# Kernel optimization log

Hardware: AMD Instinct MI355X
Metric: run time of the kernel (lower is better)

The kernel has to match this reference:

```python
import jax, jax.numpy as jnp
import numpy as np

# Intrinsics from innerProdLoss defaults
FX, FY, CX, CY = 48.0, 48.0, 48.0, 36.0
H, W = int(2 * CY), int(2 * CX)  # 72, 96
N = H * W                         # 6912 pixels
SIGMA2 = 1.0                      # geometric Gaussian-kernel bandwidth (reconstructed kern_mat)
EPS = 1e-8


def make_yz1_grid():
    # K = [[cx,fx,0],[cy,0,fy],[1,0,0]]; yz1_grid = inv(K) @ uv1_grid, shape [3, N]
    K = np.array([[CX, FX, 0.0], [CY, 0.0, FY], [1.0, 0.0, 0.0]], dtype=np.float64)
    invK = np.linalg.inv(K).astype(np.float32)
    u = np.arange(W, dtype=np.float32)
    v = np.arange(H, dtype=np.float32)
    uu = np.tile(u[None, :], (H, 1)).reshape(-1)
    vv = np.tile(v[:, None], (1, W)).reshape(-1)
    uv1 = np.stack([uu, vv, np.ones_like(uu)], axis=0)  # [3, N]
    return jnp.asarray(invK @ uv1)

YZ1 = make_yz1_grid()  # [3, N]


def kern_mat(p1, p2):
    # p1, p2: [B, 3, N] point clouds -> [B, N, N] Gaussian kernel exp(-||d||^2 / (2 sigma^2)).
    # Squared distances via norms + cross term (no [B,3,N,N] diff tensor).
    n1 = jnp.sum(p1 * p1, axis=1)                    # [B, N]
    n2 = jnp.sum(p2 * p2, axis=1)                    # [B, N]
    cross = jnp.einsum('bcm,bcn->bmn', p1, p2)       # [B, N, N]
    d2 = jnp.maximum(n1[:, :, None] + n2[:, None, :] - 2.0 * cross, 0.0)
    return jnp.exp(-d2 / (2.0 * SIGMA2))


def gramian(f1, f2):
    # f1, f2: [B, C, H, W] -> gramian [B, N, N] of L2-normalized features (norm_mode=1, kernalize=False).
    B, C, Hh, Ww = f1.shape
    n = Hh * Ww
    f1 = f1.reshape(B, C, n)
    f2 = f2.reshape(B, C, n)
    norm1 = jnp.linalg.norm(f1, axis=1)              # [B, N]
    norm2 = jnp.linalg.norm(f2, axis=1)
    fea_norm_sum = jnp.sum(norm1) + jnp.sum(norm2)
    f1n = f1 / (norm1[:, None, :] + EPS)
    f2n = f2 / (norm2[:, None, :] + EPS)
    gram = jnp.einsum('bcm,bcn->bmn', f1n, f2n) / n  # norm_mode=1 normalization
    return gram, fea_norm_sum


def setup_inputs() -> dict:
    key = jax.random.key(0)
    k1, k2, k3, k4, k5 = jax.random.split(key, 5)
    B, C = 1, 16
    feature1 = jax.random.normal(k1, (B, C, H, W), jnp.float32)
    feature2 = jax.random.normal(k2, (B, C, H, W), jnp.float32)
    depth1 = jax.random.uniform(k3, (B, 1, H, W), jnp.float32, 0.5, 5.0)
    depth2 = jax.random.uniform(k4, (B, 1, H, W), jnp.float32, 0.5, 5.0)
    pose1_2 = jnp.tile(jnp.eye(4, dtype=jnp.float32)[None], (B, 1, 1))
    pose_noise = jnp.eye(4, dtype=jnp.float32) + 0.01 * jax.random.normal(k5, (4, 4), jnp.float32)
    return {"feature1": feature1, "feature2": feature2, "depth1": depth1,
            "depth2": depth2, "pose1_2": pose1_2, "pose_noise": pose_noise}


def reference(feature1, feature2, depth1, depth2, pose1_2, pose_noise):
    B = depth1.shape[0]
    # gen_3D: back-project pixels using depth
    xyz1 = YZ1[None] * depth1.reshape(B, 1, N)       # [B, 3, N]
    xyz2 = YZ1[None] * depth2.reshape(B, 1, N)
    xyz2_homo = jnp.concatenate([xyz2, jnp.ones((B, 1, N), xyz2.dtype)], axis=1)  # [B, 4, N]
    xyz2_trans = jnp.matmul(pose1_2, xyz2_homo)[:, :3, :]

    gram_feat, fea_norm_sum = gramian(feature1, feature2)
    pcl_diff_exp = kern_mat(xyz1, xyz2_trans)

    # L2_norm=True, diff_mode=True -> scale by 100
    fea_norm_sum = fea_norm_sum * 100.0

    # diff_mode: noisy pose branch
    pose_noisy = jnp.matmul(pose1_2, pose_noise)
    xyz2_trans_noisy = jnp.matmul(pose_noisy, xyz2_homo)[:, :3, :]
    pcl_diff_exp_noisy = kern_mat(xyz1, xyz2_trans_noisy)

    inner_neg = -jnp.sum((pcl_diff_exp - pcl_diff_exp_noisy) * gram_feat)
    final_loss = inner_neg  # sparse_mode=False
    return final_loss, inner_neg, fea_norm_sum
```

## Files before the change

### kernel.cpp

```cpp
#include <hip/hip_runtime.h>
#include <math.h>

#define NPIX 6912
#define LOG2E 1.4426950408889634f

typedef __fp16 v8h  __attribute__((ext_vector_type(8)));
typedef float  v16f __attribute__((ext_vector_type(16)));

#define OFF_ROWFEAT 0
#define OFF_ROWGEO  221184
#define OFF_COLFEAT 442368
#define OFF_COLB1   663552
#define OFF_COLB2   884736
#define OFF_PART    1105920
#define OFF_NPART   1117584
#define NPART_BLOCKS 2916
#define NNORM_BLOCKS 108

__device__ __forceinline__ float fast_exp2(float x) { return __builtin_amdgcn_exp2f(x); }

__device__ __forceinline__ float wave_reduce_64(float v) {
    #pragma unroll
    for (int o = 32; o > 0; o >>= 1) v += __shfl_down(v, o, 64);
    return v;
}

__device__ __forceinline__ float block_reduce_256(float v, float* smem4) {
    __syncthreads();
    v = wave_reduce_64(v);
    const int lane = threadIdx.x & 63;
    const int w = threadIdx.x >> 6;
    if (lane == 0) smem4[w] = v;
    __syncthreads();
    float r = 0.0f;
    if (threadIdx.x == 0) r = smem4[0] + smem4[1] + smem4[2] + smem4[3];
    return r;
}

__device__ __forceinline__ void split_hl(float x, __fp16& h, __fp16& l) {
    h = (__fp16)x;
    l = (__fp16)(x - (float)h);
}

__global__ __launch_bounds__(64)
void preproc_kernel(const float* __restrict__ f1, const float* __restrict__ f2,
                    const float* __restrict__ d1, const float* __restrict__ d2,
                    const float* __restrict__ pose, const float* __restrict__ pnz,
                    char* __restrict__ wsb) {
    const int i = blockIdx.x * 64 + threadIdx.x;

    __fp16* rowfeat = (__fp16*)(wsb + OFF_ROWFEAT);
    __fp16* rowgeo  = (__fp16*)(wsb + OFF_ROWGEO);
    __fp16* colfeat = (__fp16*)(wsb + OFF_COLFEAT);
    __fp16* colB1   = (__fp16*)(wsb + OFF_COLB1);
    __fp16* colB2   = (__fp16*)(wsb + OFF_COLB2);
    float*  npart   = (float*)(wsb + OFF_NPART);

    float P[12];
    #pragma unroll
    for (int k = 0; k < 12; k++) P[k] = pose[k];
    float Q[12];
    #pragma unroll
    for (int r = 0; r < 3; r++) {
        #pragma unroll
        for (int c = 0; c < 4; c++) {
            float s = 0.0f;
            #pragma unroll
            for (int k = 0; k < 4; k++) s = fmaf(pose[r * 4 + k], pnz[k * 4 + c], s);
            Q[r * 4 + c] = s;
        }
    }

    const float inv48 = 1.0f / 48.0f;
    const int u = i % 96;
    const int v = i / 96;
    const float y1 = fmaf((float)u, inv48, -1.0f);
    const float y2 = fmaf((float)v, inv48, -0.75f);

    const float dep1 = d1[i];
    const float px = dep1, py = y1 * dep1, pz = y2 * dep1;
    const float n1 = px * px + py * py + pz * pz;
    const float wlog = -0.5f * LOG2E * n1;

    const float ptx = LOG2E * px, pty = LOG2E * py, ptz = LOG2E * pz;
    __fp16 phx, phy, phz, plx, ply, plz, wh, wl;
    split_hl(ptx, phx, plx);
    split_hl(pty, phy, ply);
    split_hl(ptz, phz, plz);
    split_hl(wlog, wh, wl);
    {
        __fp16 rg[16] = {phx, phy, phz,  phx, phy, phz,  plx, ply, plz,
                         (__fp16)1.0f, (__fp16)1.0f, wh, wl,
                         (__fp16)0, (__fp16)0, (__fp16)0};
        *(v8h*)(rowgeo + (size_t)i * 16)     = *(v8h*)(rg);
        *(v8h*)(rowgeo + (size_t)i * 16 + 8) = *(v8h*)(rg + 8);
    }

    const float dep2 = d2[i];
    const float a = dep2, b = y1 * dep2, g = y2 * dep2;
    const float t0 = P[0] * a + P[1] * b + P[2]  * g + P[3];
    const float t1 = P[4] * a + P[5] * b + P[6]  * g + P[7];
    const float t2 = P[8] * a + P[9] * b + P[10] * g + P[11];
    const float q0 = Q[0] * a + Q[1] * b + Q[2]  * g + Q[3];
    const float q1 = Q[4] * a + Q[5] * b + Q[6]  * g + Q[7];
    const float q2 = Q[8] * a + Q[9] * b + Q[10] * g + Q[11];
    const float nt = t0 * t0 + t1 * t1 + t2 * t2;
    const float nq = q0 * q0 + q1 * q1 + q2 * q2;
    const float cA = -0.5f * LOG2E * nt;
    const float dc = 0.5f * LOG2E * (nt - nq);

    __fp16 thx, thy, thz, tlx, tly, tlz, cAh, cAl, dch, dcl;
    split_hl(t0, thx, tlx);
    split_hl(t1, thy, tly);
    split_hl(t2, thz, tlz);
    split_hl(cA, cAh, cAl);
    split_hl(dc, dch, dcl);
    {
        __fp16 b1a[16] = {thx, thy, thz,  tlx, tly, tlz,  thx, thy, thz,
                          cAh, cAl, (__fp16)1.0f, (__fp16)1.0f,
                          (__fp16)0, (__fp16)0, (__fp16)0};
        *(v8h*)(colB1 + (size_t)i * 16)     = *(v8h*)(b1a);
        *(v8h*)(colB1 + (size_t)i * 16 + 8) = *(v8h*)(b1a + 8);
    }
    const __fp16 dtx = (__fp16)(q0 - t0), dty = (__fp16)(q1 - t1), dtz = (__fp16)(q2 - t2);
    {
        __fp16 b2a[16] = {dtx, dty, dtz,  (__fp16)0, (__fp16)0, (__fp16)0,  dtx, dty, dtz,
                          dch, dcl, (__fp16)0, (__fp16)0,
                          (__fp16)0, (__fp16)0, (__fp16)0};
        *(v8h*)(colB2 + (size_t)i * 16)     = *(v8h*)(b2a);
        *(v8h*)(colB2 + (size_t)i * 16 + 8) = *(v8h*)(b2a + 8);
    }

    float s1 = 0.0f, s2 = 0.0f;
    float v1[16], v2[16];
    #pragma unroll
    for (int cc = 0; cc < 16; cc++) {
        v1[cc] = f1[cc * NPIX + i];
        v2[cc] = f2[cc * NPIX + i];
        s1 = fmaf(v1[cc], v1[cc], s1);
        s2 = fmaf(v2[cc], v2[cc], s2);
    }
    const float nrm1 = sqrtf(s1), nrm2 = sqrtf(s2);
    const float r1 = 1.0f / (nrm1 + 1e-8f), r2 = 1.0f / (nrm2 + 1e-8f);
    {
        __fp16 rf[16], cf[16];
        #pragma unroll
        for (int cc = 0; cc < 16; cc++) {
            rf[cc] = (__fp16)(v1[cc] * r1);
            cf[cc] = (__fp16)(v2[cc] * r2);
        }
        *(v8h*)(rowfeat + (size_t)i * 16)     = *(v8h*)(rf);
        *(v8h*)(rowfeat + (size_t)i * 16 + 8) = *(v8h*)(rf + 8);
        *(v8h*)(colfeat + (size_t)i * 16)     = *(v8h*)(cf);
        *(v8h*)(colfeat + (size_t)i * 16 + 8) = *(v8h*)(cf + 8);
    }

    float tot = wave_reduce_64(nrm1 + nrm2);
    if (threadIdx.x == 0) npart[blockIdx.x] = tot;
}

__global__ __launch_bounds__(256)
void pair_kernel(const char* __restrict__ wsb) {
    __shared__ float smem4[4];

    const __fp16* rowfeat = (const __fp16*)(wsb + OFF_ROWFEAT);
    const __fp16* rowgeo  = (const __fp16*)(wsb + OFF_ROWGEO);
    const __fp16* colfeat = (const __fp16*)(wsb + OFF_COLFEAT);
    const __fp16* colB1   = (const __fp16*)(wsb + OFF_COLB1);
    const __fp16* colB2   = (const __fp16*)(wsb + OFF_COLB2);
    float*        part    = (float*)(const_cast<char*>(wsb) + OFF_PART);

    const int t = threadIdx.x;
    const int w = t >> 6;
    const int L = t & 63;
    const int c31 = L & 31;
    const int kh8 = (L >> 5) * 8;

    const int arow = blockIdx.y * 128 + w * 32 + c31;
    const v8h afeat = *(const v8h*)(rowfeat + (size_t)arow * 16 + kh8);
    const v8h ageo  = *(const v8h*)(rowgeo  + (size_t)arow * 16 + kh8);

    const int cbase = blockIdx.x * 128;
    const size_t boff0 = (size_t)(cbase + c31) * 16 + kh8;

    float acc0 = 0.0f, acc1 = 0.0f;
    v8h bf = *(const v8h*)(colfeat + boff0);
    v8h b1 = *(const v8h*)(colB1   + boff0);
    v8h b2 = *(const v8h*)(colB2   + boff0);

    #pragma unroll
    for (int ct = 0; ct < 4; ct++) {
        v8h nbf, nb1, nb2;
        if (ct < 3) {
            const size_t noff = boff0 + (size_t)(ct + 1) * 32 * 16;
            nbf = *(const v8h*)(colfeat + noff);
            nb1 = *(const v8h*)(colB1   + noff);
            nb2 = *(const v8h*)(colB2   + noff);
        }

        v16f z = {};
        const v16f dotv = __builtin_amdgcn_mfma_f32_32x32x16_f16(afeat, bf, z, 0, 0, 0);
        const v16f a1v  = __builtin_amdgcn_mfma_f32_32x32x16_f16(ageo,  b1, z, 0, 0, 0);
        const v16f dlv  = __builtin_amdgcn_mfma_f32_32x32x16_f16(ageo,  b2, z, 0, 0, 0);

        #pragma unroll
        for (int i = 0; i < 8; i++) {
            const float e1a = fast_exp2(a1v[i]);
            const float e2a = fast_exp2(a1v[i] + dlv[i]);
            const float e1b = fast_exp2(a1v[i + 8]);
            const float e2b = fast_exp2(a1v[i + 8] + dlv[i + 8]);
            acc0 = fmaf(e1a - e2a, dotv[i], acc0);
            acc1 = fmaf(e1b - e2b, dotv[i + 8], acc1);
        }
        if (ct < 3) { bf = nbf; b1 = nb1; b2 = nb2; }
    }

    float v = wave_reduce_64(acc0 + acc1);
    if (L == 0) smem4[w] = v;
    __syncthreads();
    if (t == 0)
        part[blockIdx.y * 54 + blockIdx.x] = smem4[0] + smem4[1] + smem4[2] + smem4[3];
}

__global__ __launch_bounds__(256)
void finalize_kernel(const char* __restrict__ wsb, float* __restrict__ out) {
    __shared__ float smem4[4];
    const float* part  = (const float*)(wsb + OFF_PART);
    const float* npart = (const float*)(wsb + OFF_NPART);
    const int t = threadIdx.x;

    float s = 0.0f;
    for (int i = t; i < NPART_BLOCKS; i += 256) s += part[i];
    const float tot = block_reduce_256(s, smem4);

    float ns = (t < NNORM_BLOCKS) ? npart[t] : 0.0f;
    const float ntot = block_reduce_256(ns, smem4);

    if (t == 0) {
        const float vc = -tot * (1.0f / (float)NPIX);
        out[0] = vc;
        out[1] = vc;
        out[2] = 100.0f * ntot;
    }
}

extern "C" void kernel_launch(void* const* d_in, const int* in_sizes, int n_in,
                              void* d_out, int out_size, void* d_ws, size_t ws_size,
                              hipStream_t stream) {
    const float* feature1 = (const float*)d_in[0];
    const float* feature2 = (const float*)d_in[1];
    const float* depth1   = (const float*)d_in[2];
    const float* depth2   = (const float*)d_in[3];
    const float* pose1_2  = (const float*)d_in[4];
    const float* posenz   = (const float*)d_in[5];
    float* out = (float*)d_out;
    char*  wsb = (char*)d_ws;

    preproc_kernel<<<108, 64, 0, stream>>>(feature1, feature2, depth1, depth2,
                                           pose1_2, posenz, wsb);
    dim3 grid(54, 54);
    pair_kernel<<<grid, 256, 0, stream>>>(wsb);
    finalize_kernel<<<1, 256, 0, stream>>>(wsb, out);
}
```

Before: 86.02 us.

## Fuse preprocessing into pair kernel with per-block LDS recomputation

Removes the separate preprocessing kernel. Each pair block instead computes its own 128 row and 128 column operand tiles (normalized features, geometry split into half precision) directly from the inputs and stores them in shared memory. This removes one kernel launch and the workspace write/read round trip, and lets the MFMA loop read B operands from LDS. In exchange, every block redundantly recomputes and reloads its tiles from global memory, and the feature-norm partials are now reduced across all blocks.

```diff
diff --git a/kernel.cpp b/kernel.cpp
--- a/kernel.cpp
+++ b/kernel.cpp
@@ -7,15 +7,10 @@
 typedef __fp16 v8h  __attribute__((ext_vector_type(8)));
 typedef float  v16f __attribute__((ext_vector_type(16)));
 
-#define OFF_ROWFEAT 0
-#define OFF_ROWGEO  221184
-#define OFF_COLFEAT 442368
-#define OFF_COLB1   663552
-#define OFF_COLB2   884736
-#define OFF_PART    1105920
-#define OFF_NPART   1117584
+#define OFF_PART    0
+#define OFF_NPART   11664
+#define NLB 54
 #define NPART_BLOCKS 2916
-#define NNORM_BLOCKS 108
 
 __device__ __forceinline__ float fast_exp2(float x) { return __builtin_amdgcn_exp2f(x); }
 
@@ -42,161 +37,166 @@
     l = (__fp16)(x - (float)h);
 }
 
-__global__ __launch_bounds__(64)
-void preproc_kernel(const float* __restrict__ f1, const float* __restrict__ f2,
-                    const float* __restrict__ d1, const float* __restrict__ d2,
-                    const float* __restrict__ pose, const float* __restrict__ pnz,
-                    char* __restrict__ wsb) {
-    const int i = blockIdx.x * 64 + threadIdx.x;
-
-    __fp16* rowfeat = (__fp16*)(wsb + OFF_ROWFEAT);
-    __fp16* rowgeo  = (__fp16*)(wsb + OFF_ROWGEO);
-    __fp16* colfeat = (__fp16*)(wsb + OFF_COLFEAT);
-    __fp16* colB1   = (__fp16*)(wsb + OFF_COLB1);
-    __fp16* colB2   = (__fp16*)(wsb + OFF_COLB2);
-    float*  npart   = (float*)(wsb + OFF_NPART);
-
-    float P[12];
-    #pragma unroll
-    for (int k = 0; k < 12; k++) P[k] = pose[k];
-    float Q[12];
-    #pragma unroll
-    for (int r = 0; r < 3; r++) {
-        #pragma unroll
-        for (int c = 0; c < 4; c++) {
-            float s = 0.0f;
+__global__ __launch_bounds__(256)
+void pair_kernel(const float* __restrict__ f1, const float* __restrict__ f2,
+                 const float* __restrict__ d1, const float* __restrict__ d2,
+                 const float* __restrict__ pose, const float* __restrict__ pnz,
+                 char* __restrict__ wsb) {
+    __shared__ __align__(16) __fp16 srowfeat[128 * 16];
+    __shared__ __align__(16) __fp16 srowgeo [128 * 16];
+    __shared__ __align__(16) __fp16 scolfeat[128 * 16];
+    __shared__ __align__(16) __fp16 scolB1  [128 * 16];
+    __shared__ __align__(16) __fp16 scolB2  [128 * 16];
+    __shared__ float smem4[4];
+
+    float* part  = (float*)(wsb + OFF_PART);
+    float* npart = (float*)(wsb + OFF_NPART);
+
+    const int t  = threadIdx.x;
+    const int bx = blockIdx.x;
+    const int by = blockIdx.y;
+
+    const float inv48 = 1.0f / 48.0f;
+    float nsum = 0.0f;
+
+    if (t < 128) {
+        const int i = by * 128 + t;
+        const int u = i % 96, v = i / 96;
+        const float y1 = fmaf((float)u, inv48, -1.0f);
+        const float y2 = fmaf((float)v, inv48, -0.75f);
+
+        const float dep1 = d1[i];
+        const float px = dep1, py = y1 * dep1, pz = y2 * dep1;
+        const float n1 = px * px + py * py + pz * pz;
+        const float wlog = -0.5f * LOG2E * n1;
+
+        const float ptx = LOG2E * px, pty = LOG2E * py, ptz = LOG2E * pz;
+        __fp16 phx, phy, phz, plx, ply, plz, wh, wl;
+        split_hl(ptx, phx, plx);
+        split_hl(pty, phy, ply);
+        split_hl(ptz, phz, plz);
+        split_hl(wlog, wh, wl);
+        {
+            __fp16 rg[16] = {phx, phy, phz,  phx, phy, phz,  plx, ply, plz,
+                             (__fp16)1.0f, (__fp16)1.0f, wh, wl,
+                             (__fp16)0, (__fp16)0, (__fp16)0};
+            *(v8h*)(srowgeo + t * 16)     = *(v8h*)(rg);
+            *(v8h*)(srowgeo + t * 16 + 8) = *(v8h*)(rg + 8);
+        }
+
+        float s1 = 0.0f;
+        float v1[16];
+        #pragma unroll
+        for (int cc = 0; cc < 16; cc++) {
+            v1[cc] = f1[cc * NPIX + i];
+            s1 = fmaf(v1[cc], v1[cc], s1);
+        }
+        const float nrm1 = sqrtf(s1);
+        const float r1 = 1.0f / (nrm1 + 1e-8f);
+        {
+            __fp16 rf[16];
             #pragma unroll
-            for (int k = 0; k < 4; k++) s = fmaf(pose[r * 4 + k], pnz[k * 4 + c], s);
-            Q[r * 4 + c] = s;
-        }
-    }
-
-    const float inv48 = 1.0f / 48.0f;
-    const int u = i % 96;
-    const int v = i / 96;
-    const float y1 = fmaf((float)u, inv48, -1.0f);
-    const float y2 = fmaf((float)v, inv48, -0.75f);
-
-    const float dep1 = d1[i];
-    const float px = dep1, py = y1 * dep1, pz = y2 * dep1;
-    const float n1 = px * px + py * py + pz * pz;
-    const float wlog = -0.5f * LOG2E * n1;
-
-    const float ptx = LOG2E * px, pty = LOG2E * py, ptz = LOG2E * pz;
-    __fp16 phx, phy, phz, plx, ply, plz, wh, wl;
-    split_hl(ptx, phx, plx);
-    split_hl(pty, phy, ply);
-    split_hl(ptz, phz, plz);
-    split_hl(wlog, wh, wl);
-    {
-        __fp16 rg[16] = {phx, phy, phz,  phx, phy, phz,  plx, ply, plz,
-                         (__fp16)1.0f, (__fp16)1.0f, wh, wl,
-                         (__fp16)0, (__fp16)0, (__fp16)0};
-        *(v8h*)(rowgeo + (size_t)i * 16)     = *(v8h*)(rg);
-        *(v8h*)(rowgeo + (size_t)i * 16 + 8) = *(v8h*)(rg + 8);
-    }
-
-    const float dep2 = d2[i];
-    const float a = dep2, b = y1 * dep2, g = y2 * dep2;
-    const float t0 = P[0] * a + P[1] * b + P[2]  * g + P[3];
-    const float t1 = P[4] * a + P[5] * b + P[6]  * g + P[7];
-    const float t2 = P[8] * a + P[9] * b + P[10] * g + P[11];
-    const float q0 = Q[0] * a + Q[1] * b + Q[2]  * g + Q[3];
-    const float q1 = Q[4] * a + Q[5] * b + Q[6]  * g + Q[7];
-    const float q2 = Q[8] * a + Q[9] * b + Q[10] * g + Q[11];
-    const float nt = t0 * t0 + t1 * t1 + t2 * t2;
-    const float nq = q0 * q0 + q1 * q1 + q2 * q2;
-    const float cA = -0.5f * LOG2E * nt;
-    const float dc = 0.5f * LOG2E * (nt - nq);
-
-    __fp16 thx, thy, thz, tlx, tly, tlz, cAh, cAl, dch, dcl;
-    split_hl(t0, thx, tlx);
-    split_hl(t1, thy, tly);
-    split_hl(t2, thz, tlz);
-    split_hl(cA, cAh, cAl);
-    split_hl(dc, dch, dcl);
-    {
-        __fp16 b1a[16] = {thx, thy, thz,  tlx, tly, tlz,  thx, thy, thz,
-                          cAh, cAl, (__fp16)1.0f, (__fp16)1.0f,
-                          (__fp16)0, (__fp16)0, (__fp16)0};
-        *(v8h*)(colB1 + (size_t)i * 16)     = *(v8h*)(b1a);
-        *(v8h*)(colB1 + (size_t)i * 16 + 8) = *(v8h*)(b1a + 8);
-    }
-    const __fp16 dtx = (__fp16)(q0 - t0), dty = (__fp16)(q1 - t1), dtz = (__fp16)(q2 - t2);
-    {
-        __fp16 b2a[16] = {dtx, dty, dtz,  (__fp16)0, (__fp16)0, (__fp16)0,  dtx, dty, dtz,
-                          dch, dcl, (__fp16)0, (__fp16)0,
-                          (__fp16)0, (__fp16)0, (__fp16)0};
-        *(v8h*)(colB2 + (size_t)i * 16)     = *(v8h*)(b2a);
-        *(v8h*)(colB2 + (size_t)i * 16 + 8) = *(v8h*)(b2a + 8);
-    }
-
-    float s1 = 0.0f, s2 = 0.0f;
-    float v1[16], v2[16];
-    #pragma unroll
-    for (int cc = 0; cc < 16; cc++) {
-        v1[cc] = f1[cc * NPIX + i];
-        v2[cc] = f2[cc * NPIX + i];
-        s1 = fmaf(v1[cc], v1[cc], s1);
-        s2 = fmaf(v2[cc], v2[cc], s2);
-    }
-    const float nrm1 = sqrtf(s1), nrm2 = sqrtf(s2);
-    const float r1 = 1.0f / (nrm1 + 1e-8f), r2 = 1.0f / (nrm2 + 1e-8f);
-    {
-        __fp16 rf[16], cf[16];
+            for (int cc = 0; cc < 16; cc++) rf[cc] = (__fp16)(v1[cc] * r1);
+            *(v8h*)(srowfeat + t * 16)     = *(v8h*)(rf);
+            *(v8h*)(srowfeat + t * 16 + 8) = *(v8h*)(rf + 8);
+        }
+        if (bx == 0) nsum = nrm1;
+    } else {
+        const int c = t - 128;
+        const int n = bx * 128 + c;
+        const int u = n % 96, v = n / 96;
+        const float y1 = fmaf((float)u, inv48, -1.0f);
+        const float y2 = fmaf((float)v, inv48, -0.75f);
+
+        float P[12];
+        #pragma unroll
+        for (int k = 0; k < 12; k++) P[k] = pose[k];
+        float Q[12];
+        #pragma unroll
+        for (int r = 0; r < 3; r++) {
+            #pragma unroll
+            for (int cq = 0; cq < 4; cq++) {
+                float s = 0.0f;
+                #pragma unroll
+                for (int k = 0; k < 4; k++) s = fmaf(pose[r * 4 + k], pnz[k * 4 + cq], s);
+                Q[r * 4 + cq] = s;
+            }
+        }
+
+        const float dep2 = d2[n];
+        const float a = dep2, b = y1 * dep2, g = y2 * dep2;
+        const float t0 = P[0] * a + P[1] * b + P[2]  * g + P[3];
+        const float t1 = P[4] * a + P[5] * b + P[6]  * g + P[7];
+        const float t2 = P[8] * a + P[9] * b + P[10] * g + P[11];
+        const float q0 = Q[0] * a + Q[1] * b + Q[2]  * g + Q[3];
+        const float q1 = Q[4] * a + Q[5] * b + Q[6]  * g + Q[7];
+        const float q2 = Q[8] * a + Q[9] * b + Q[10] * g + Q[11];
+        const float nt = t0 * t0 + t1 * t1 + t2 * t2;
+        const float nq = q0 * q0 + q1 * q1 + q2 * q2;
+        const float cA = -0.5f * LOG2E * nt;
+        const float dc = 0.5f * LOG2E * (nt - nq);
+
+        __fp16 thx, thy, thz, tlx, tly, tlz, cAh, cAl, dch, dcl;
+        split_hl(t0, thx, tlx);
+        split_hl(t1, thy, tly);
+        split_hl(t2, thz, tlz);
+        split_hl(cA, cAh, cAl);
+        split_hl(dc, dch, dcl);
+
+        float s2 = 0.0f;
+        float v2[16];
         #pragma unroll
         for (int cc = 0; cc < 16; cc++) {
-            rf[cc] = (__fp16)(v1[cc] * r1);
-            cf[cc] = (__fp16)(v2[cc] * r2);
-        }
-        *(v8h*)(rowfeat + (size_t)i * 16)     = *(v8h*)(rf);
-        *(v8h*)(rowfeat + (size_t)i * 16 + 8) = *(v8h*)(rf + 8);
-        *(v8h*)(colfeat + (size_t)i * 16)     = *(v8h*)(cf);
-        *(v8h*)(colfeat + (size_t)i * 16 + 8) = *(v8h*)(cf + 8);
-    }
-
-    float tot = wave_reduce_64(nrm1 + nrm2);
-    if (threadIdx.x == 0) npart[blockIdx.x] = tot;
-}
-
-__global__ __launch_bounds__(256)
-void pair_kernel(const char* __restrict__ wsb) {
-    __shared__ float smem4[4];
-
-    const __fp16* rowfeat = (const __fp16*)(wsb + OFF_ROWFEAT);
-    const __fp16* rowgeo  = (const __fp16*)(wsb + OFF_ROWGEO);
-    const __fp16* colfeat = (const __fp16*)(wsb + OFF_COLFEAT);
-    const __fp16* colB1   = (const __fp16*)(wsb + OFF_COLB1);
-    const __fp16* colB2   = (const __fp16*)(wsb + OFF_COLB2);
-    float*        part    = (float*)(const_cast<char*>(wsb) + OFF_PART);
-
-    const int t = threadIdx.x;
-    const int w = t >> 6;
-    const int L = t & 63;
+            v2[cc] = f2[cc * NPIX + n];
+            s2 = fmaf(v2[cc], v2[cc], s2);
+        }
+        const float nrm2 = sqrtf(s2);
+        const float r2 = 1.0f / (nrm2 + 1e-8f);
+
+        const int g0 = (c >> 5) * 64 + (c & 31);
+        {
+            __fp16 cf[16];
+            #pragma unroll
+            for (int cc = 0; cc < 16; cc++) cf[cc] = (__fp16)(v2[cc] * r2);
+            *(v8h*)(scolfeat + g0 * 8)        = *(v8h*)(cf);
+            *(v8h*)(scolfeat + (g0 + 32) * 8) = *(v8h*)(cf + 8);
+        }
+        {
+            __fp16 b1a[16] = {thx, thy, thz,  tlx, tly, tlz,  thx, thy, thz,
+                              cAh, cAl, (__fp16)1.0f, (__fp16)1.0f,
+                              (__fp16)0, (__fp16)0, (__fp16)0};
+            *(v8h*)(scolB1 + g0 * 8)        = *(v8h*)(b1a);
+            *(v8h*)(scolB1 + (g0 + 32) * 8) = *(v8h*)(b1a + 8);
+        }
+        const __fp16 dtx = (__fp16)(q0 - t0), dty = (__fp16)(q1 - t1), dtz = (__fp16)(q2 - t2);
+        {
+            __fp16 b2a[16] = {dtx, dty, dtz,  (__fp16)0, (__fp16)0, (__fp16)0,  dtx, dty, dtz,
+                              dch, dcl, (__fp16)0, (__fp16)0,
+                              (__fp16)0, (__fp16)0, (__fp16)0};
+            *(v8h*)(scolB2 + g0 * 8)        = *(v8h*)(b2a);
+            *(v8h*)(scolB2 + (g0 + 32) * 8) = *(v8h*)(b2a + 8);
+        }
+        if (by == 0) nsum = nrm2;
+    }
+
+    __syncthreads();
+
+    const int w   = t >> 6;
+    const int L   = t & 63;
     const int c31 = L & 31;
     const int kh8 = (L >> 5) * 8;
 
-    const int arow = blockIdx.y * 128 + w * 32 + c31;
-    const v8h afeat = *(const v8h*)(rowfeat + (size_t)arow * 16 + kh8);
-    const v8h ageo  = *(const v8h*)(rowgeo  + (size_t)arow * 16 + kh8);
-
-    const int cbase = blockIdx.x * 128;
-    const size_t boff0 = (size_t)(cbase + c31) * 16 + kh8;
+    const int arowl = w * 32 + c31;
+    const v8h afeat = *(const v8h*)(srowfeat + arowl * 16 + kh8);
+    const v8h ageo  = *(const v8h*)(srowgeo  + arowl * 16 + kh8);
 
     float acc0 = 0.0f, acc1 = 0.0f;
-    v8h bf = *(const v8h*)(colfeat + boff0);
-    v8h b1 = *(const v8h*)(colB1   + boff0);
-    v8h b2 = *(const v8h*)(colB2   + boff0);
-
     #pragma unroll
     for (int ct = 0; ct < 4; ct++) {
-        v8h nbf, nb1, nb2;
-        if (ct < 3) {
-            const size_t noff = boff0 + (size_t)(ct + 1) * 32 * 16;
-            nbf = *(const v8h*)(colfeat + noff);
-            nb1 = *(const v8h*)(colB1   + noff);
-            nb2 = *(const v8h*)(colB2   + noff);
-        }
+        const int off = (ct * 64 + L) * 8;
+        const v8h bf = *(const v8h*)(scolfeat + off);
+        const v8h b1 = *(const v8h*)(scolB1 + off);
+        const v8h b2 = *(const v8h*)(scolB2 + off);
 
         v16f z = {};
         const v16f dotv = __builtin_amdgcn_mfma_f32_32x32x16_f16(afeat, bf, z, 0, 0, 0);
@@ -212,14 +212,19 @@
             acc0 = fmaf(e1a - e2a, dotv[i], acc0);
             acc1 = fmaf(e1b - e2b, dotv[i + 8], acc1);
         }
-        if (ct < 3) { bf = nbf; b1 = nb1; b2 = nb2; }
-    }
-
-    float v = wave_reduce_64(acc0 + acc1);
-    if (L == 0) smem4[w] = v;
-    __syncthreads();
-    if (t == 0)
-        part[blockIdx.y * 54 + blockIdx.x] = smem4[0] + smem4[1] + smem4[2] + smem4[3];
+    }
+
+    {
+        const float v = wave_reduce_64(acc0 + acc1);
+        if (L == 0) smem4[w] = v;
+        __syncthreads();
+        if (t == 0)
+            part[by * NLB + bx] = smem4[0] + smem4[1] + smem4[2] + smem4[3];
+    }
+    {
+        const float v = block_reduce_256(nsum, smem4);
+        if (t == 0) npart[by * NLB + bx] = v;
+    }
 }
 
 __global__ __launch_bounds__(256)
@@ -233,7 +238,8 @@
     for (int i = t; i < NPART_BLOCKS; i += 256) s += part[i];
     const float tot = block_reduce_256(s, smem4);
 
-    float ns = (t < NNORM_BLOCKS) ? npart[t] : 0.0f;
+    float ns = 0.0f;
+    for (int i = t; i < NPART_BLOCKS; i += 256) ns += npart[i];
     const float ntot = block_reduce_256(ns, smem4);
 
     if (t == 0) {
@@ -256,9 +262,8 @@
     float* out = (float*)d_out;
     char*  wsb = (char*)d_ws;
 
-    preproc_kernel<<<108, 64, 0, stream>>>(feature1, feature2, depth1, depth2,
-                                           pose1_2, posenz, wsb);
-    dim3 grid(54, 54);
-    pair_kernel<<<grid, 256, 0, stream>>>(wsb);
+    dim3 grid(NLB, NLB);
+    pair_kernel<<<grid, 256, 0, stream>>>(feature1, feature2, depth1, depth2,
+                                          pose1_2, posenz, wsb);
     finalize_kernel<<<1, 256, 0, stream>>>(wsb, out);
 }
```

Result: slower. 90.92 us (+5.7%).
